# Optimization experiments

Hardware: AMD Instinct MI355X
Metric: run time of the kernel (lower is better)

## Reference

```python
import jax, jax.numpy as jnp
import numpy as np

N_EMBED = 1024
N_HEADS = 16
CTX = 2048
B, T = 4, 2048
HD = N_EMBED // N_HEADS


def setup_inputs() -> dict:
    key = jax.random.key(0)
    ks = jax.random.split(key, 5)
    scale = 1.0 / np.sqrt(N_EMBED)
    return {
        "x": jax.random.normal(ks[0], (B, T, N_EMBED), dtype=jnp.float32),
        "wq": jax.random.normal(ks[1], (N_EMBED, N_EMBED), dtype=jnp.float32) * scale,
        "wk": jax.random.normal(ks[2], (N_EMBED, N_EMBED), dtype=jnp.float32) * scale,
        "wv": jax.random.normal(ks[3], (N_EMBED, N_EMBED), dtype=jnp.float32) * scale,
        "wo": jax.random.normal(ks[4], (N_EMBED, N_EMBED), dtype=jnp.float32) * scale,
    }


def reference(x, wq, wk, wv, wo):
    b, t, c = x.shape
    # nn.Linear applies x @ W.T ; split heads -> [B, H, T, hd]
    def proj(w):
        return jnp.einsum("btc,dc->btd", x, w).reshape(b, t, N_HEADS, HD).transpose(0, 2, 1, 3)
    q, k, v = proj(wq), proj(wk), proj(wv)
    scores = jnp.einsum("bhqd,bhkd->bhqk", q, k) * (HD ** -0.5)
    causal = jnp.tril(jnp.ones((t, t), dtype=bool))
    scores = jnp.where(causal[None, None, :, :], scores, -jnp.inf)
    a = jax.nn.softmax(scores, axis=-1)
    o = jnp.einsum("bhqk,bhkd->bhqd", a, v)  # [B,H,T,hd]
    o = o.transpose(0, 2, 1, 3).reshape(b, t, c)
    return jnp.einsum("btc,dc->btd", o, wo)
```

## Files before the change

kernel.cpp:

```cpp
#include <hip/hip_runtime.h>
#include <stdint.h>


typedef __attribute__((ext_vector_type(8))) short bf16x8;
typedef __attribute__((ext_vector_type(4))) float f32x4;
typedef unsigned short us;

#define LOG2E 1.4426950408889634f

#define GL2LDS16(g, l)                                                          \
  __builtin_amdgcn_global_load_lds(                                             \
      (const __attribute__((address_space(1))) unsigned int*)(g),               \
      (__attribute__((address_space(3))) unsigned int*)(l), 16, 0, 0)

__device__ inline us f2bf(float f) {
  union { float f; unsigned int u; } v; v.f = f;
  unsigned int u = v.u;
  u += 0x7FFFu + ((u >> 16) & 1u);
  return (us)(u >> 16);
}

__global__ void cast_all(const float* __restrict__ x,
                         const float* __restrict__ w0, const float* __restrict__ w1,
                         const float* __restrict__ w2, const float* __restrict__ w3,
                         us* __restrict__ xb, us* __restrict__ wbuf) {
  int i = (blockIdx.x * blockDim.x + threadIdx.x) * 8;
  const float* src;
  us* dst;
  float sc = 1.0f;
  if (i < (8 << 20)) {
    src = x + i; dst = xb + i;
  } else {
    int j = i - (8 << 20);
    int seg = j >> 20;
    int off = j & ((1 << 20) - 1);
    const float* w = (seg == 0) ? w0 : (seg == 1) ? w1 : (seg == 2) ? w2 : w3;
    if (seg == 0) sc = 0.125f * LOG2E;
    src = w + off; dst = wbuf + j;
  }
  float4 a = *reinterpret_cast<const float4*>(src);
  float4 b = *reinterpret_cast<const float4*>(src + 4);
  union { us u[8]; uint4 v; } o;
  o.u[0] = f2bf(a.x * sc); o.u[1] = f2bf(a.y * sc);
  o.u[2] = f2bf(a.z * sc); o.u[3] = f2bf(a.w * sc);
  o.u[4] = f2bf(b.x * sc); o.u[5] = f2bf(b.y * sc);
  o.u[6] = f2bf(b.z * sc); o.u[7] = f2bf(b.w * sc);
  *reinterpret_cast<uint4*>(dst) = o.v;
}

__global__ __launch_bounds__(256, 2) void gemm_qkv(
    const us* __restrict__ A, const us* __restrict__ Bw,
    us* __restrict__ QKV, us* __restrict__ Vt) {
  const int K = 1024, N = 3072;
  __shared__ __align__(16) us Al[128 * 64];
  __shared__ __align__(16) us Bl[128 * 64];
  const int tid = threadIdx.x;
  const int lane = tid & 63;
  const int w = tid >> 6;
  const int quad = lane >> 4;
  const int l16 = lane & 15;
  const int m0 = blockIdx.y * 128;
  const int n0 = blockIdx.x * 128;
  const int wm = w >> 1, wn = w & 1;
  const int srow_base = w * 8 + (lane >> 3);
  const int sunit = lane & 7;
  f32x4 acc[4][4] = {};

  for (int k0 = 0; k0 < K; k0 += 64) {
    __syncthreads();
#pragma unroll
    for (int it = 0; it < 4; ++it) {
      int row = it * 32 + srow_base;
      int gu = sunit ^ (row & 7);
      int base = __builtin_amdgcn_readfirstlane((it * 256 + w * 64) * 8);
      GL2LDS16(A + (size_t)(m0 + row) * K + k0 + gu * 8, &Al[base]);
      GL2LDS16(Bw + (size_t)(n0 + row) * K + k0 + gu * 8, &Bl[base]);
    }
    __syncthreads();
#pragma unroll
    for (int kk = 0; kk < 2; ++kk) {
      bf16x8 af[4], bfr[4];
#pragma unroll
      for (int mi = 0; mi < 4; ++mi) {
        int row = wm * 64 + mi * 16 + l16;
        af[mi] = *reinterpret_cast<const bf16x8*>(
            &Al[row * 64 + (((kk * 4 + quad) ^ (row & 7)) * 8)]);
      }
#pragma unroll
      for (int ni = 0; ni < 4; ++ni) {
        int row = wn * 64 + ni * 16 + l16;
        bfr[ni] = *reinterpret_cast<const bf16x8*>(
            &Bl[row * 64 + (((kk * 4 + quad) ^ (row & 7)) * 8)]);
      }
#pragma unroll
      for (int mi = 0; mi < 4; ++mi)
#pragma unroll
        for (int ni = 0; ni < 4; ++ni)
          acc[mi][ni] = __builtin_amdgcn_mfma_f32_16x16x32_bf16(af[mi], bfr[ni], acc[mi][ni], 0, 0, 0);
    }
  }

  if (n0 < 2048) {
#pragma unroll
    for (int mi = 0; mi < 4; ++mi)
#pragma unroll
      for (int ni = 0; ni < 4; ++ni)
#pragma unroll
        for (int r = 0; r < 4; ++r) {
          int row = m0 + wm * 64 + mi * 16 + quad * 4 + r;
          int col = n0 + wn * 64 + ni * 16 + l16;
          QKV[(size_t)row * N + col] = f2bf(acc[mi][ni][r]);
        }
  } else {
    const int b = m0 >> 11;
    const int kt = ((m0 & 2047) >> 6) + wm;
#pragma unroll
    for (int mi = 0; mi < 4; ++mi)
#pragma unroll
      for (int ni = 0; ni < 4; ++ni)
#pragma unroll
        for (int r = 0; r < 4; ++r) {
          int col = n0 + wn * 64 + ni * 16 + l16;
          int h = (col - 2048) >> 6;
          int d = col & 63;
          int sj = (quad * 4 + r) * 4 + mi;
          Vt[((size_t)((b * 16 + h) * 64 + d)) * 2048 + kt * 64 + sj] = f2bf(acc[mi][ni][r]);
        }
  }
}

__global__ __launch_bounds__(256, 2) void gemm_out(
    const us* __restrict__ A, const us* __restrict__ Bw,
    float* __restrict__ Cv, int M, int N, int K) {
  __shared__ __align__(16) us Al[128 * 64];
  __shared__ __align__(16) us Bl[128 * 64];
  const int tid = threadIdx.x;
  const int lane = tid & 63;
  const int w = tid >> 6;
  const int quad = lane >> 4;
  const int l16 = lane & 15;
  const int m0 = blockIdx.y * 128;
  const int n0 = blockIdx.x * 128;
  const int wm = w >> 1, wn = w & 1;
  const int srow_base = w * 8 + (lane >> 3);
  const int sunit = lane & 7;
  f32x4 acc[4][4] = {};

  for (int k0 = 0; k0 < K; k0 += 64) {
    __syncthreads();
#pragma unroll
    for (int it = 0; it < 4; ++it) {
      int row = it * 32 + srow_base;
      int gu = sunit ^ (row & 7);
      int base = __builtin_amdgcn_readfirstlane((it * 256 + w * 64) * 8);
      GL2LDS16(A + (size_t)(m0 + row) * K + k0 + gu * 8, &Al[base]);
      GL2LDS16(Bw + (size_t)(n0 + row) * K + k0 + gu * 8, &Bl[base]);
    }
    __syncthreads();
#pragma unroll
    for (int kk = 0; kk < 2; ++kk) {
      bf16x8 af[4], bfr[4];
#pragma unroll
      for (int mi = 0; mi < 4; ++mi) {
        int row = wm * 64 + mi * 16 + l16;
        af[mi] = *reinterpret_cast<const bf16x8*>(
            &Al[row * 64 + (((kk * 4 + quad) ^ (row & 7)) * 8)]);
      }
#pragma unroll
      for (int ni = 0; ni < 4; ++ni) {
        int row = wn * 64 + ni * 16 + l16;
        bfr[ni] = *reinterpret_cast<const bf16x8*>(
            &Bl[row * 64 + (((kk * 4 + quad) ^ (row & 7)) * 8)]);
      }
#pragma unroll
      for (int mi = 0; mi < 4; ++mi)
#pragma unroll
        for (int ni = 0; ni < 4; ++ni)
          acc[mi][ni] = __builtin_amdgcn_mfma_f32_16x16x32_bf16(af[mi], bfr[ni], acc[mi][ni], 0, 0, 0);
    }
  }

#pragma unroll
  for (int mi = 0; mi < 4; ++mi)
#pragma unroll
    for (int ni = 0; ni < 4; ++ni)
#pragma unroll
      for (int r = 0; r < 4; ++r) {
        int row = m0 + wm * 64 + mi * 16 + quad * 4 + r;
        int col = n0 + wn * 64 + ni * 16 + l16;
        Cv[(size_t)row * N + col] = acc[mi][ni][r];
      }
}

__global__ __launch_bounds__(512, 6) void attn(
    const us* __restrict__ QKV, const us* __restrict__ Vt,
    us* __restrict__ O) {
  __shared__ __align__(16) us Kb[2][64 * 64];
  __shared__ __align__(16) us Vb[2][64 * 64];
  __shared__ __align__(16) us Pl[8][16 * 64];
  const int bid = blockIdx.x;
  const int qt = 15 - (bid >> 6);
  const int bh = bid & 63;
  const int b = bh >> 4, h = bh & 15;
  const int q0 = qt * 128;
  const int tid = threadIdx.x, lane = tid & 63, w = tid >> 6;
  const int quad = lane >> 4, l16 = lane & 15;
  const size_t rowbase = (size_t)b * 2048;
  const int qcol = h * 64;
  const int kcol = 1024 + h * 64;
  const int qrow = q0 + w * 16;
  const int nT = 2 * qt + 2;

  const bf16x8 ones = {(short)0x3F80, (short)0x3F80, (short)0x3F80, (short)0x3F80,
                       (short)0x3F80, (short)0x3F80, (short)0x3F80, (short)0x3F80};

  bf16x8 qf[2];
#pragma unroll
  for (int dc = 0; dc < 2; ++dc)
    qf[dc] = *reinterpret_cast<const bf16x8*>(
        &QKV[(rowbase + qrow + l16) * 3072 + qcol + dc * 32 + quad * 8]);

  f32x4 oacc[4] = {};
  f32x4 lacc = {};

  const int rr = tid >> 3;
  const int gu = (tid & 7) ^ (rr & 7);
  const int sbase = __builtin_amdgcn_readfirstlane(w * 512);

  auto stage = [&](int kt, int buf) {
    GL2LDS16(QKV + (rowbase + kt * 64 + rr) * 3072 + kcol + gu * 8,
             &Kb[buf][0] + sbase);
    GL2LDS16(Vt + ((size_t)((b * 16 + h) * 64 + rr)) * 2048 + kt * 64 + gu * 8,
             &Vb[buf][0] + sbase);
  };

  stage(0, 0);

  for (int kt = 0; kt < nT; ++kt) {
    asm volatile("s_waitcnt vmcnt(0)" ::: "memory");
    asm volatile("s_barrier" ::: "memory");
    if (kt + 1 < nT) stage(kt + 1, (kt + 1) & 1);
    const us* Kl = &Kb[kt & 1][0];
    const us* Vl = &Vb[kt & 1][0];

    const int kdiff = qrow + 15 - kt * 64;
    if (kdiff < 0) continue;
    const int tmax = (kdiff >= 48) ? 4 : ((kdiff >> 4) + 1);

    f32x4 s[4];
    float p[4][4];
#pragma unroll
    for (int t = 0; t < 4; ++t) {
      if (t < tmax) {
        s[t] = f32x4{0.f, 0.f, 0.f, 0.f};
        int krow = t * 16 + l16;
#pragma unroll
        for (int dc = 0; dc < 2; ++dc) {
          bf16x8 kf = *reinterpret_cast<const bf16x8*>(
              &Kl[krow * 64 + (((dc * 4 + quad) ^ (l16 & 7)) * 8)]);
          s[t] = __builtin_amdgcn_mfma_f32_16x16x32_bf16(qf[dc], kf, s[t], 0, 0, 0);
        }
      }
    }
    const bool do_mask = (kt * 64 + 63) > qrow;
#pragma unroll
    for (int t = 0; t < 4; ++t) {
      if (t < tmax) {
        if (do_mask) {
#pragma unroll
          for (int r = 0; r < 4; ++r) {
            float e = __builtin_amdgcn_exp2f(s[t][r]);
            int kg = kt * 64 + t * 16 + l16;
            int qgl = qrow + quad * 4 + r;
            p[t][r] = (kg <= qgl) ? e : 0.f;
          }
        } else {
#pragma unroll
          for (int r = 0; r < 4; ++r)
            p[t][r] = __builtin_amdgcn_exp2f(s[t][r]);
        }
      } else {
#pragma unroll
        for (int r = 0; r < 4; ++r) p[t][r] = 0.f;
      }
    }
#pragma unroll
    for (int r = 0; r < 4; ++r) {
      int prow = quad * 4 + r;
      uint2 val;
      val.x = __builtin_amdgcn_perm(__float_as_uint(p[1][r]), __float_as_uint(p[0][r]), 0x07060302u);
      val.y = __builtin_amdgcn_perm(__float_as_uint(p[3][r]), __float_as_uint(p[2][r]), 0x07060302u);
      char* dst = (char*)&Pl[w][0] + prow * 128 +
                  (((l16 >> 1) ^ (prow & 7)) * 16) + (l16 & 1) * 8;
      *reinterpret_cast<uint2*>(dst) = val;
    }
    asm volatile("s_waitcnt lgkmcnt(0)" ::: "memory");
#pragma unroll
    for (int kc = 0; kc < 2; ++kc) {
      bf16x8 pf = *reinterpret_cast<const bf16x8*>(
          (const char*)&Pl[w][0] + l16 * 128 + (((kc * 4 + quad) ^ (l16 & 7)) * 16));
      lacc = __builtin_amdgcn_mfma_f32_16x16x32_bf16(pf, ones, lacc, 0, 0, 0);
#pragma unroll
      for (int dt = 0; dt < 4; ++dt) {
        bf16x8 vf = *reinterpret_cast<const bf16x8*>(
            &Vl[(dt * 16 + l16) * 64 + (((kc * 4 + quad) ^ (l16 & 7)) * 8)]);
        oacc[dt] = __builtin_amdgcn_mfma_f32_16x16x32_bf16(pf, vf, oacc[dt], 0, 0, 0);
      }
    }
  }

#pragma unroll
  for (int dt = 0; dt < 4; ++dt)
#pragma unroll
    for (int r = 0; r < 4; ++r) {
      int row = qrow + quad * 4 + r;
      O[(rowbase + row) * 1024 + qcol + dt * 16 + l16] = f2bf(oacc[dt][r] / lacc[r]);
    }
}

extern "C" void kernel_launch(void* const* d_in, const int* in_sizes, int n_in,
                              void* d_out, int out_size, void* d_ws, size_t ws_size,
                              hipStream_t stream) {
  const float* x = (const float*)d_in[0];
  const float* wq = (const float*)d_in[1];
  const float* wk = (const float*)d_in[2];
  const float* wv = (const float*)d_in[3];
  const float* wo = (const float*)d_in[4];

  const int BT = 8192, E = 1024;
  const size_t NX = (size_t)BT * E;
  const size_t NW = (size_t)E * E;

  us* xb = (us*)d_ws;
  us* wbuf = xb + NX;
  us* QKV = wbuf + 4 * NW;
  us* VtB = QKV + (size_t)BT * 3 * E;
  us* Ob = xb;

  cast_all<<<(int)((NX + 4 * NW) / 8 / 256), 256, 0, stream>>>(x, wq, wk, wv, wo, xb, wbuf);

  gemm_qkv<<<dim3(24, 64), 256, 0, stream>>>(xb, wbuf, QKV, VtB);
  attn<<<1024, 512, 0, stream>>>(QKV, VtB, Ob);
  gemm_out<<<dim3(8, 64), 256, 0, stream>>>(Ob, wbuf + 3 * NW, (float*)d_out, BT, E, E);
}
```

Measured before the change: 232.8 us.

## Rewrite attention with 32x32 MFMA and register-resident P via permlane swap

The attention kernel moves from 16x16x32 to 32x32x16 bf16 MFMA, with 4 waves of 32 query rows each instead of 8 waves of 16. Scores are computed transposed (K as the A operand), so exp'd probabilities can be packed with v_cvt_pk_bf16_f32 and rearranged across lanes with v_permlane32_swap. This removes the per-wave LDS round trip for P. The V-transpose store in the QKV GEMM is changed to a plain row-natural layout, and query tiles are reordered across the grid to balance causal work. The trade-off is higher register pressure from 16-element accumulators and fewer threads per block.

Result: slower. 252.8 us (+8.6%).

```diff
diff --git a/kernel.cpp b/kernel.cpp
--- a/kernel.cpp
+++ b/kernel.cpp
@@ -4,7 +4,9 @@
 
 typedef __attribute__((ext_vector_type(8))) short bf16x8;
 typedef __attribute__((ext_vector_type(4))) float f32x4;
+typedef __attribute__((ext_vector_type(16))) float f32x16;
 typedef unsigned short us;
+typedef unsigned int u32;
 
 #define LOG2E 1.4426950408889634f
 
@@ -112,19 +114,19 @@
           QKV[(size_t)row * N + col] = f2bf(acc[mi][ni][r]);
         }
   } else {
-    const int b = m0 >> 11;
-    const int kt = ((m0 & 2047) >> 6) + wm;
+    const int bI = m0 >> 11;
+    const int tbase = m0 & 2047;
 #pragma unroll
     for (int mi = 0; mi < 4; ++mi)
 #pragma unroll
       for (int ni = 0; ni < 4; ++ni)
 #pragma unroll
         for (int r = 0; r < 4; ++r) {
+          int krow = tbase + wm * 64 + mi * 16 + quad * 4 + r;
           int col = n0 + wn * 64 + ni * 16 + l16;
-          int h = (col - 2048) >> 6;
+          int hh = (col - 2048) >> 6;
           int d = col & 63;
-          int sj = (quad * 4 + r) * 4 + mi;
-          Vt[((size_t)((b * 16 + h) * 64 + d)) * 2048 + kt * 64 + sj] = f2bf(acc[mi][ni][r]);
+          Vt[((size_t)((bI * 16 + hh) * 64 + d)) * 2048 + krow] = f2bf(acc[mi][ni][r]);
         }
   }
 }
@@ -192,46 +194,53 @@
       }
 }
 
-__global__ __launch_bounds__(512, 6) void attn(
+__global__ __launch_bounds__(256, 4) void attn(
     const us* __restrict__ QKV, const us* __restrict__ Vt,
     us* __restrict__ O) {
   __shared__ __align__(16) us Kb[2][64 * 64];
   __shared__ __align__(16) us Vb[2][64 * 64];
-  __shared__ __align__(16) us Pl[8][16 * 64];
   const int bid = blockIdx.x;
-  const int qt = 15 - (bid >> 6);
+  const int j16 = bid >> 6;
+  const int grp = j16 >> 2, pos = j16 & 3;
+  const int qt = (grp == 0) ? 15 - pos : (grp == 1) ? pos
+               : (grp == 2) ? 11 - pos : 4 + pos;
   const int bh = bid & 63;
   const int b = bh >> 4, h = bh & 15;
   const int q0 = qt * 128;
   const int tid = threadIdx.x, lane = tid & 63, w = tid >> 6;
-  const int quad = lane >> 4, l16 = lane & 15;
+  const int l31 = lane & 31, hi = lane >> 5;
   const size_t rowbase = (size_t)b * 2048;
   const int qcol = h * 64;
   const int kcol = 1024 + h * 64;
-  const int qrow = q0 + w * 16;
+  const int qw = q0 + w * 32;
   const int nT = 2 * qt + 2;
 
   const bf16x8 ones = {(short)0x3F80, (short)0x3F80, (short)0x3F80, (short)0x3F80,
                        (short)0x3F80, (short)0x3F80, (short)0x3F80, (short)0x3F80};
 
-  bf16x8 qf[2];
-#pragma unroll
-  for (int dc = 0; dc < 2; ++dc)
-    qf[dc] = *reinterpret_cast<const bf16x8*>(
-        &QKV[(rowbase + qrow + l16) * 3072 + qcol + dc * 32 + quad * 8]);
-
-  f32x4 oacc[4] = {};
-  f32x4 lacc = {};
-
-  const int rr = tid >> 3;
-  const int gu = (tid & 7) ^ (rr & 7);
-  const int sbase = __builtin_amdgcn_readfirstlane(w * 512);
+  bf16x8 qf[4];
+#pragma unroll
+  for (int ds = 0; ds < 4; ++ds)
+    qf[ds] = *reinterpret_cast<const bf16x8*>(
+        &QKV[(rowbase + qw + l31) * 3072 + qcol + ds * 16 + hi * 8]);
+
+  f32x16 oacc[2] = {};
+  f32x16 lacc = {};
+
+  const int rr8 = w * 8 + (lane >> 3);
+  const int uu = lane & 7;
 
   auto stage = [&](int kt, int buf) {
-    GL2LDS16(QKV + (rowbase + kt * 64 + rr) * 3072 + kcol + gu * 8,
-             &Kb[buf][0] + sbase);
-    GL2LDS16(Vt + ((size_t)((b * 16 + h) * 64 + rr)) * 2048 + kt * 64 + gu * 8,
-             &Vb[buf][0] + sbase);
+#pragma unroll
+    for (int c = 0; c < 2; ++c) {
+      int row = c * 32 + rr8;
+      int gu = uu ^ (row & 7);
+      int base = __builtin_amdgcn_readfirstlane((c * 32 + w * 8) * 64);
+      GL2LDS16(QKV + (rowbase + kt * 64 + row) * 3072 + kcol + gu * 8,
+               &Kb[buf][base]);
+      GL2LDS16(Vt + ((size_t)(bh * 64 + row)) * 2048 + kt * 64 + gu * 8,
+               &Vb[buf][base]);
+    }
   };
 
   stage(0, 0);
@@ -243,78 +252,90 @@
     const us* Kl = &Kb[kt & 1][0];
     const us* Vl = &Vb[kt & 1][0];
 
-    const int kdiff = qrow + 15 - kt * 64;
+    const int kdiff = qw + 31 - kt * 64;
     if (kdiff < 0) continue;
-    const int tmax = (kdiff >= 48) ? 4 : ((kdiff >> 4) + 1);
-
-    f32x4 s[4];
-    float p[4][4];
-#pragma unroll
-    for (int t = 0; t < 4; ++t) {
+    const int tmax = (kdiff >= 32) ? 2 : 1;
+    const bool do_mask = (kt * 64 + 63) > qw;
+
+    f32x16 s[2] = {};
+#pragma unroll
+    for (int t = 0; t < 2; ++t) {
       if (t < tmax) {
-        s[t] = f32x4{0.f, 0.f, 0.f, 0.f};
-        int krow = t * 16 + l16;
-#pragma unroll
-        for (int dc = 0; dc < 2; ++dc) {
+#pragma unroll
+        for (int ds = 0; ds < 4; ++ds) {
+          int row = t * 32 + l31;
           bf16x8 kf = *reinterpret_cast<const bf16x8*>(
-              &Kl[krow * 64 + (((dc * 4 + quad) ^ (l16 & 7)) * 8)]);
-          s[t] = __builtin_amdgcn_mfma_f32_16x16x32_bf16(qf[dc], kf, s[t], 0, 0, 0);
-        }
-      }
-    }
-    const bool do_mask = (kt * 64 + 63) > qrow;
-#pragma unroll
-    for (int t = 0; t < 4; ++t) {
+              &Kl[row * 64 + (((ds * 2 + hi) ^ (row & 7)) * 8)]);
+          s[t] = __builtin_amdgcn_mfma_f32_32x32x16_bf16(kf, qf[ds], s[t], 0, 0, 0);
+        }
+      }
+    }
+
+    u32 pa[4][4];
+#pragma unroll
+    for (int t = 0; t < 2; ++t) {
       if (t < tmax) {
+        float p[16];
         if (do_mask) {
 #pragma unroll
-          for (int r = 0; r < 4; ++r) {
+          for (int r = 0; r < 16; ++r) {
             float e = __builtin_amdgcn_exp2f(s[t][r]);
-            int kg = kt * 64 + t * 16 + l16;
-            int qgl = qrow + quad * 4 + r;
-            p[t][r] = (kg <= qgl) ? e : 0.f;
+            int kg = kt * 64 + t * 32 + (r & 3) + ((r >> 2) << 3) + hi * 4;
+            p[r] = (kg <= qw + l31) ? e : 0.f;
           }
         } else {
 #pragma unroll
-          for (int r = 0; r < 4; ++r)
-            p[t][r] = __builtin_amdgcn_exp2f(s[t][r]);
-        }
-      } else {
-#pragma unroll
-        for (int r = 0; r < 4; ++r) p[t][r] = 0.f;
-      }
-    }
-#pragma unroll
-    for (int r = 0; r < 4; ++r) {
-      int prow = quad * 4 + r;
-      uint2 val;
-      val.x = __builtin_amdgcn_perm(__float_as_uint(p[1][r]), __float_as_uint(p[0][r]), 0x07060302u);
-      val.y = __builtin_amdgcn_perm(__float_as_uint(p[3][r]), __float_as_uint(p[2][r]), 0x07060302u);
-      char* dst = (char*)&Pl[w][0] + prow * 128 +
-                  (((l16 >> 1) ^ (prow & 7)) * 16) + (l16 & 1) * 8;
-      *reinterpret_cast<uint2*>(dst) = val;
-    }
-    asm volatile("s_waitcnt lgkmcnt(0)" ::: "memory");
-#pragma unroll
-    for (int kc = 0; kc < 2; ++kc) {
-      bf16x8 pf = *reinterpret_cast<const bf16x8*>(
-          (const char*)&Pl[w][0] + l16 * 128 + (((kc * 4 + quad) ^ (l16 & 7)) * 16));
-      lacc = __builtin_amdgcn_mfma_f32_16x16x32_bf16(pf, ones, lacc, 0, 0, 0);
-#pragma unroll
-      for (int dt = 0; dt < 4; ++dt) {
-        bf16x8 vf = *reinterpret_cast<const bf16x8*>(
-            &Vl[(dt * 16 + l16) * 64 + (((kc * 4 + quad) ^ (l16 & 7)) * 8)]);
-        oacc[dt] = __builtin_amdgcn_mfma_f32_16x16x32_bf16(pf, vf, oacc[dt], 0, 0, 0);
-      }
-    }
-  }
-
-#pragma unroll
-  for (int dt = 0; dt < 4; ++dt)
-#pragma unroll
-    for (int r = 0; r < 4; ++r) {
-      int row = qrow + quad * 4 + r;
-      O[(rowbase + row) * 1024 + qcol + dt * 16 + l16] = f2bf(oacc[dt][r] / lacc[r]);
+          for (int r = 0; r < 16; ++r) p[r] = __builtin_amdgcn_exp2f(s[t][r]);
+        }
+        u32 pk[4][2];
+#pragma unroll
+        for (int bb = 0; bb < 4; ++bb)
+#pragma unroll
+          for (int w2 = 0; w2 < 2; ++w2)
+            asm("v_cvt_pk_bf16_f32 %0, %1, %2"
+                : "=v"(pk[bb][w2])
+                : "v"(p[4 * bb + 2 * w2]), "v"(p[4 * bb + 2 * w2 + 1]));
+#pragma unroll
+        for (int s2 = 0; s2 < 2; ++s2)
+#pragma unroll
+          for (int w2 = 0; w2 < 2; ++w2) {
+            u32 a = pk[2 * s2][w2];
+            u32 c = pk[2 * s2 + 1][w2];
+            asm volatile("v_permlane32_swap_b32 %0, %1" : "+v"(a), "+v"(c));
+            pa[t * 2 + s2][w2] = a;
+            pa[t * 2 + s2][2 + w2] = c;
+          }
+      }
+    }
+
+#pragma unroll
+    for (int ks = 0; ks < 4; ++ks) {
+      if (ks < tmax * 2) {
+        union { u32 u[4]; bf16x8 v; } pu;
+        pu.u[0] = pa[ks][0]; pu.u[1] = pa[ks][1];
+        pu.u[2] = pa[ks][2]; pu.u[3] = pa[ks][3];
+        bf16x8 paf = pu.v;
+        lacc = __builtin_amdgcn_mfma_f32_32x32x16_bf16(paf, ones, lacc, 0, 0, 0);
+#pragma unroll
+        for (int dt = 0; dt < 2; ++dt) {
+          int row = dt * 32 + l31;
+          bf16x8 vf = *reinterpret_cast<const bf16x8*>(
+              &Vl[row * 64 + (((ks * 2 + hi) ^ (row & 7)) * 8)]);
+          oacc[dt] = __builtin_amdgcn_mfma_f32_32x32x16_bf16(paf, vf, oacc[dt], 0, 0, 0);
+        }
+      }
+    }
+  }
+
+  float inv[16];
+#pragma unroll
+  for (int r = 0; r < 16; ++r) inv[r] = 1.0f / lacc[r];
+#pragma unroll
+  for (int dt = 0; dt < 2; ++dt)
+#pragma unroll
+    for (int r = 0; r < 16; ++r) {
+      int qg = qw + (r & 3) + ((r >> 2) << 3) + hi * 4;
+      O[(rowbase + qg) * 1024 + qcol + dt * 32 + l31] = f2bf(oacc[dt][r] * inv[r]);
     }
 }
 
@@ -340,6 +361,6 @@
   cast_all<<<(int)((NX + 4 * NW) / 8 / 256), 256, 0, stream>>>(x, wq, wk, wv, wo, xb, wbuf);
 
   gemm_qkv<<<dim3(24, 64), 256, 0, stream>>>(xb, wbuf, QKV, VtB);
-  attn<<<1024, 512, 0, stream>>>(QKV, VtB, Ob);
+  attn<<<1024, 256, 0, stream>>>(QKV, VtB, Ob);
   gemm_out<<<dim3(8, 64), 256, 0, stream>>>(Ob, wbuf + 3 * NW, (float*)d_out, BT, E, E);
 }
```
